# Kernel tuning notes

Measured on AMD Instinct MI355X. Metric: run time of the kernel, lower is better.

## Reference

```python
import jax, jax.numpy as jnp
import numpy as np

B = 4096
NUM_FEATURES = 2048
NUM_NEURONS = 1024
NUM_TARGETS = 8
NNZ1 = 65536
NNZ2 = 8192


def _sparse_linear(x, w, b, rows, cols, n_out):
    """y[b, o] = sum_{e: rows[e]==o} w[e] * x[b, cols[e]] + b[o].

    x: [B, n_in], w: [nnz], rows/cols: [nnz] int, b: [n_out].
    """
    prod = x[:, cols] * w  # [B, nnz] gather + elementwise
    # segment_sum reduces over leading axis -> work on [nnz, B]
    y = jax.ops.segment_sum(prod.T, rows, num_segments=n_out)  # [n_out, B]
    return y.T + b


def setup_inputs() -> dict:
    key = jax.random.key(0)
    ks = jax.random.split(key, 9)
    x = jax.random.normal(ks[0], (B, NUM_FEATURES), dtype=jnp.float32)
    w1 = jax.random.normal(ks[1], (NNZ1,), dtype=jnp.float32) * 0.05
    b1 = jax.random.normal(ks[2], (NUM_NEURONS,), dtype=jnp.float32) * 0.05
    w2 = jax.random.normal(ks[3], (NNZ2,), dtype=jnp.float32) * 0.05
    b2 = jax.random.normal(ks[4], (NUM_TARGETS,), dtype=jnp.float32) * 0.05
    conn1_out = jax.random.randint(ks[5], (NNZ1,), 0, NUM_NEURONS, dtype=jnp.int64 if jax.config.jax_enable_x64 else jnp.int32)
    conn1_in = jax.random.randint(ks[6], (NNZ1,), 0, NUM_FEATURES, dtype=conn1_out.dtype)
    conn2_out = jax.random.randint(ks[7], (NNZ2,), 0, NUM_TARGETS, dtype=conn1_out.dtype)
    conn2_in = jax.random.randint(ks[8], (NNZ2,), 0, NUM_NEURONS, dtype=conn1_out.dtype)
    return {
        "x": x, "w1": w1, "b1": b1, "w2": w2, "b2": b2,
        "conn1_out": conn1_out, "conn1_in": conn1_in,
        "conn2_out": conn2_out, "conn2_in": conn2_in,
    }


def reference(x, w1, b1, w2, b2, conn1_out, conn1_in, conn2_out, conn2_in):
    h = jax.nn.sigmoid(_sparse_linear(x, w1, b1, conn1_out, conn1_in, b1.shape[0]))
    out = _sparse_linear(h, w2, b2, conn2_out, conn2_in, b2.shape[0])
    # num_targets = 8 != 1, so no final sigmoid (matches CrossEntropyLoss path)
    return out
```

## Files before the change

kernel.cpp:

```cpp
#include <hip/hip_runtime.h>
#include <math.h>

#define BATCH 4096
#define NFEAT 2048
#define NNEUR 1024
#define NTGT  8
#define NNZ1  65536
#define NNZ2  8192

#define BM 128
#define BN 64
#define BK 64
#define KSTEPS (NFEAT / BK)

typedef short  bf16x8 __attribute__((ext_vector_type(8)));
typedef float  f32x4  __attribute__((ext_vector_type(4)));

#define OFF_W1F  ((size_t)0)
#define OFF_W2D  ((size_t)8388608)
#define OFF_W1B  ((size_t)8421376)

#define ZERO_FLOAT4 526336
#define OUT_FLOAT4  (BATCH * NTGT / 4)

__device__ __forceinline__ unsigned short f2bf(float f) {
    union { float f; unsigned int u; } a; a.f = f;
    unsigned int u = a.u;
    u += 0x7fffu + ((u >> 16) & 1u);
    return (unsigned short)(u >> 16);
}

__device__ __forceinline__ uint4 pk8(float4 lo, float4 hi) {
    uint4 r;
    asm("v_cvt_pk_bf16_f32 %0, %1, %2" : "=v"(r.x) : "v"(lo.x), "v"(lo.y));
    asm("v_cvt_pk_bf16_f32 %0, %1, %2" : "=v"(r.y) : "v"(lo.z), "v"(lo.w));
    asm("v_cvt_pk_bf16_f32 %0, %1, %2" : "=v"(r.z) : "v"(hi.x), "v"(hi.y));
    asm("v_cvt_pk_bf16_f32 %0, %1, %2" : "=v"(r.w) : "v"(hi.z), "v"(hi.w));
    return r;
}

__global__ void k_zero(float4* __restrict__ ws4, float4* __restrict__ out4,
                       const float* __restrict__ b2) {
    int i = blockIdx.x * blockDim.x + threadIdx.x;
    if (i < ZERO_FLOAT4) {
        ws4[i] = make_float4(0.f, 0.f, 0.f, 0.f);
    } else {
        int j = i - ZERO_FLOAT4;
        if (j < OUT_FLOAT4) {
            int p = (j & 1) * 4;
            out4[j] = make_float4(b2[p], b2[p + 1], b2[p + 2], b2[p + 3]);
        }
    }
}

__global__ void k_build(const float* __restrict__ w1, const int* __restrict__ c1o,
                        const int* __restrict__ c1i,
                        const float* __restrict__ w2, const int* __restrict__ c2o,
                        const int* __restrict__ c2i,
                        float* __restrict__ W1f, float* __restrict__ W2d) {
    int i = blockIdx.x * blockDim.x + threadIdx.x;
    if (i < NNZ1) {
        atomicAdd(&W1f[(size_t)c1o[i] * NFEAT + c1i[i]], w1[i]);
    } else {
        int j = i - NNZ1;
        if (j < NNZ2) atomicAdd(&W2d[c2i[j] * NTGT + c2o[j]], w2[j]);
    }
}

__global__ void k_convert(const float* __restrict__ W1f, unsigned short* __restrict__ W1b) {
    int i = blockIdx.x * blockDim.x + threadIdx.x;
    float4 v = ((const float4*)W1f)[i];
    ushort4 o;
    o.x = f2bf(v.x); o.y = f2bf(v.y); o.z = f2bf(v.z); o.w = f2bf(v.w);
    ((ushort4*)W1b)[i] = o;
}

__global__ __launch_bounds__(256) void k_gemm(const unsigned short* __restrict__ W1b,
                                              const float* __restrict__ x,
                                              const float* __restrict__ b1,
                                              const float* __restrict__ W2d,
                                              float* __restrict__ out) {
    __shared__ unsigned short ldsA[2][BM * BK];
    __shared__ unsigned short ldsB[2][BN * BK];
    __shared__ float s_w2[BM][NTGT];
    __shared__ float s_b1[BM];
    __shared__ float s_pt[2][BN][NTGT];

    int bid = blockIdx.x;
    int v   = bid >> 3;
    int n0  = ((bid & 7) * 8 + (v >> 3)) * BN;
    int mt  = v & 7;
    int m0  = mt * BM;

    int tid  = threadIdx.x;
    int wv   = tid >> 6;
    int lane = tid & 63;
    int wm = wv >> 1, wn = wv & 1;
    int lr = lane & 15, lg = lane >> 4;

    for (int i = tid; i < BM * NTGT; i += 256)
        s_w2[i >> 3][i & 7] = W2d[(m0 + (i >> 3)) * NTGT + (i & 7)];
    if (tid < BM) s_b1[tid] = b1[m0 + tid];

    f32x4 zero4 = {0.f, 0.f, 0.f, 0.f};
    f32x4 acc[4][2];
#pragma unroll
    for (int i = 0; i < 4; ++i)
#pragma unroll
        for (int j = 0; j < 2; ++j) acc[i][j] = zero4;

    int r0 = tid >> 3, s0 = tid & 7;
    const unsigned short* gA0 = &W1b[(size_t)(m0 + r0) * NFEAT + s0 * 8];
    const unsigned short* gA1 = gA0 + 32 * NFEAT;
    const unsigned short* gA2 = gA0 + 64 * NFEAT;
    const unsigned short* gA3 = gA0 + 96 * NFEAT;
    const float* gB0 = &x[(size_t)(n0 + r0) * NFEAT + s0 * 8];
    const float* gB1 = gB0 + 32 * NFEAT;
    const int iw0 = r0 * 8 + (s0 ^ (r0 & 7));
    const int iw1 = iw0 + 256, iw2 = iw0 + 512, iw3 = iw0 + 768;

    bf16x8 A0a, A0b, A0c, A0d;  float4 B0a, B0b, B0c, B0d;
    bf16x8 A1a, A1b, A1c, A1d;  float4 B1a, B1b, B1c, B1d;
    bf16x8 af0[4], af1[4], bg0[2], bg1[2];

#define LOADS0(T) do { int kk = (T) * BK;                           \
        A0a = *(const bf16x8*)(gA0 + kk); A0b = *(const bf16x8*)(gA1 + kk); \
        A0c = *(const bf16x8*)(gA2 + kk); A0d = *(const bf16x8*)(gA3 + kk); \
        B0a = *(const float4*)(gB0 + kk); B0b = *(const float4*)(gB0 + kk + 4); \
        B0c = *(const float4*)(gB1 + kk); B0d = *(const float4*)(gB1 + kk + 4); } while (0)
#define LOADS1(T) do { int kk = (T) * BK;                           \
        A1a = *(const bf16x8*)(gA0 + kk); A1b = *(const bf16x8*)(gA1 + kk); \
        A1c = *(const bf16x8*)(gA2 + kk); A1d = *(const bf16x8*)(gA3 + kk); \
        B1a = *(const float4*)(gB0 + kk); B1b = *(const float4*)(gB0 + kk + 4); \
        B1c = *(const float4*)(gB1 + kk); B1d = *(const float4*)(gB1 + kk + 4); } while (0)

#define STORE0(BUF) do {                                            \
        bf16x8* dA = (bf16x8*)&ldsA[BUF][0];                        \
        dA[iw0] = A0a; dA[iw1] = A0b; dA[iw2] = A0c; dA[iw3] = A0d; \
        uint4* dB = (uint4*)&ldsB[BUF][0];                          \
        dB[iw0] = pk8(B0a, B0b); dB[iw1] = pk8(B0c, B0d); } while (0)
#define STORE1(BUF) do {                                            \
        bf16x8* dA = (bf16x8*)&ldsA[BUF][0];                        \
        dA[iw0] = A1a; dA[iw1] = A1b; dA[iw2] = A1c; dA[iw3] = A1d; \
        uint4* dB = (uint4*)&ldsB[BUF][0];                          \
        dB[iw0] = pk8(B1a, B1b); dB[iw1] = pk8(B1c, B1d); } while (0)

#define READF(BUF) do {                                             \
        const unsigned short* bA = ldsA[BUF];                       \
        const unsigned short* bB = ldsB[BUF];                       \
        _Pragma("unroll")                                           \
        for (int i = 0; i < 4; ++i) {                               \
            int rowa = wm * 64 + i * 16 + lr;                       \
            af0[i] = *(const bf16x8*)&bA[(rowa * 8 + ((lg)     ^ (rowa & 7))) * 8]; \
            af1[i] = *(const bf16x8*)&bA[(rowa * 8 + ((4 + lg) ^ (rowa & 7))) * 8]; \
        }                                                           \
        _Pragma("unroll")                                           \
        for (int j = 0; j < 2; ++j) {                               \
            int rowb = wn * 32 + j * 16 + lr;                       \
            bg0[j] = *(const bf16x8*)&bB[(rowb * 8 + ((lg)     ^ (rowb & 7))) * 8]; \
            bg1[j] = *(const bf16x8*)&bB[(rowb * 8 + ((4 + lg) ^ (rowb & 7))) * 8]; \
        }                                                           \
    } while (0)

#define MFMAS() do {                                                \
        _Pragma("unroll")                                           \
        for (int i = 0; i < 4; ++i)                                 \
            _Pragma("unroll")                                       \
            for (int j = 0; j < 2; ++j)                             \
                acc[i][j] = __builtin_amdgcn_mfma_f32_16x16x32_bf16(af0[i], bg0[j], acc[i][j], 0, 0, 0); \
        _Pragma("unroll")                                           \
        for (int i = 0; i < 4; ++i)                                 \
            _Pragma("unroll")                                       \
            for (int j = 0; j < 2; ++j)                             \
                acc[i][j] = __builtin_amdgcn_mfma_f32_16x16x32_bf16(af1[i], bg1[j], acc[i][j], 0, 0, 0); \
    } while (0)

#define LDSFENCE() asm volatile("s_waitcnt lgkmcnt(0)" ::: "memory")

    LOADS0(0);
    LOADS1(1);
    STORE0(0);
    LDSFENCE();
    __builtin_amdgcn_s_barrier();

#pragma unroll 1
    for (int p = 0; p < 15; ++p) {
        int e = 2 * p;
        LOADS0(e + 2);
        STORE1(1);
        READF(0);
        MFMAS();
        LDSFENCE();
        __builtin_amdgcn_s_barrier();
        LOADS1(e + 3);
        STORE0(0);
        READF(1);
        MFMAS();
        LDSFENCE();
        __builtin_amdgcn_s_barrier();
    }
    STORE1(1);
    READF(0);
    MFMAS();
    LDSFENCE();
    __builtin_amdgcn_s_barrier();
    READF(1);
    MFMAS();

#undef LOADS0
#undef LOADS1
#undef STORE0
#undef STORE1
#undef READF
#undef MFMAS
#undef LDSFENCE

    float pt[2][NTGT];
#pragma unroll
    for (int j = 0; j < 2; ++j)
#pragma unroll
        for (int t = 0; t < NTGT; ++t) pt[j][t] = 0.f;

#pragma unroll
    for (int i = 0; i < 4; ++i) {
#pragma unroll
        for (int r = 0; r < 4; ++r) {
            int ml = wm * 64 + i * 16 + lg * 4 + r;
            float bn = s_b1[ml];
#pragma unroll
            for (int j = 0; j < 2; ++j) {
                float h = 1.f / (1.f + __expf(-(acc[i][j][r] + bn)));
#pragma unroll
                for (int t = 0; t < NTGT; ++t)
                    pt[j][t] += h * s_w2[ml][t];
            }
        }
    }
#pragma unroll
    for (int j = 0; j < 2; ++j)
#pragma unroll
        for (int t = 0; t < NTGT; ++t) {
            float val = pt[j][t];
            val += __shfl_xor(val, 16, 64);
            val += __shfl_xor(val, 32, 64);
            pt[j][t] = val;
        }
    if (lg == 0) {
#pragma unroll
        for (int j = 0; j < 2; ++j) {
            int nl = wn * 32 + j * 16 + lr;
#pragma unroll
            for (int t = 0; t < NTGT; ++t)
                s_pt[wm][nl][t] = pt[j][t];
        }
    }
    __syncthreads();
    for (int idx = tid; idx < BN * NTGT; idx += 256) {
        int nl = idx >> 3, t = idx & 7;
        atomicAdd(&out[(size_t)(n0 + nl) * NTGT + t], s_pt[0][nl][t] + s_pt[1][nl][t]);
    }
}

extern "C" void kernel_launch(void* const* d_in, const int* in_sizes, int n_in,
                              void* d_out, int out_size, void* d_ws, size_t ws_size,
                              hipStream_t stream) {
    (void)in_sizes; (void)n_in; (void)out_size; (void)ws_size;
    const float* x   = (const float*)d_in[0];
    const float* w1  = (const float*)d_in[1];
    const float* b1  = (const float*)d_in[2];
    const float* w2  = (const float*)d_in[3];
    const float* b2  = (const float*)d_in[4];
    const int*   c1o = (const int*)d_in[5];
    const int*   c1i = (const int*)d_in[6];
    const int*   c2o = (const int*)d_in[7];
    const int*   c2i = (const int*)d_in[8];
    float* out = (float*)d_out;

    char* ws = (char*)d_ws;
    float*          W1f  = (float*)(ws + OFF_W1F);
    float*          W2d  = (float*)(ws + OFF_W2D);
    unsigned short* W1b  = (unsigned short*)(ws + OFF_W1B);

    k_zero<<<(ZERO_FLOAT4 + OUT_FLOAT4 + 255) / 256, 256, 0, stream>>>(
        (float4*)ws, (float4*)out, b2);

    k_build<<<(NNZ1 + NNZ2) / 256, 256, 0, stream>>>(w1, c1o, c1i, w2, c2o, c2i, W1f, W2d);

    k_convert<<<NNEUR * NFEAT / 4 / 256, 256, 0, stream>>>(W1f, W1b);

    k_gemm<<<(NNEUR / BM) * (BATCH / BN), 256, 0, stream>>>(W1b, x, b1, W2d, out);
}
```

Before: 50.41 us.

## Pre-convert x to bf16 and enlarge GEMM tile to 128x128

The input x is now converted to bf16 once in the conversion kernel, so the GEMM loads bf16 directly instead of converting fp32 to bf16 per tile in every block. The N tile grows from 64 to 128, giving each wave a 4x4 MFMA accumulator block and halving the number of times W1 is re-read. The LDS staging for w2, b1 and partial outputs is dropped in favour of direct global loads and per-wave atomics. In exchange there is an extra pass over x (read fp32, write bf16), only 256 blocks are launched, register pressure is higher, and more atomics hit the output.

```diff
diff --git a/kernel.cpp b/kernel.cpp
--- a/kernel.cpp
+++ b/kernel.cpp
@@ -9,7 +9,7 @@
 #define NNZ2  8192
 
 #define BM 128
-#define BN 64
+#define BN 128
 #define BK 64
 #define KSTEPS (NFEAT / BK)
 
@@ -19,6 +19,7 @@
 #define OFF_W1F  ((size_t)0)
 #define OFF_W2D  ((size_t)8388608)
 #define OFF_W1B  ((size_t)8421376)
+#define OFF_XB   ((size_t)12615680)
 
 #define ZERO_FLOAT4 526336
 #define OUT_FLOAT4  (BATCH * NTGT / 4)
@@ -28,15 +29,6 @@
     unsigned int u = a.u;
     u += 0x7fffu + ((u >> 16) & 1u);
     return (unsigned short)(u >> 16);
-}
-
-__device__ __forceinline__ uint4 pk8(float4 lo, float4 hi) {
-    uint4 r;
-    asm("v_cvt_pk_bf16_f32 %0, %1, %2" : "=v"(r.x) : "v"(lo.x), "v"(lo.y));
-    asm("v_cvt_pk_bf16_f32 %0, %1, %2" : "=v"(r.y) : "v"(lo.z), "v"(lo.w));
-    asm("v_cvt_pk_bf16_f32 %0, %1, %2" : "=v"(r.z) : "v"(hi.x), "v"(hi.y));
-    asm("v_cvt_pk_bf16_f32 %0, %1, %2" : "=v"(r.w) : "v"(hi.z), "v"(hi.w));
-    return r;
 }
 
 __global__ void k_zero(float4* __restrict__ ws4, float4* __restrict__ out4,
@@ -67,30 +59,38 @@
     }
 }
 
-__global__ void k_convert(const float* __restrict__ W1f, unsigned short* __restrict__ W1b) {
+__global__ void k_convert(const float* __restrict__ W1f, const float* __restrict__ x,
+                          unsigned short* __restrict__ W1b, unsigned short* __restrict__ xb) {
     int i = blockIdx.x * blockDim.x + threadIdx.x;
-    float4 v = ((const float4*)W1f)[i];
-    ushort4 o;
-    o.x = f2bf(v.x); o.y = f2bf(v.y); o.z = f2bf(v.z); o.w = f2bf(v.w);
-    ((ushort4*)W1b)[i] = o;
+    const int nW = NNEUR * NFEAT / 4;
+    const int nX = BATCH * NFEAT / 4;
+    if (i < nW) {
+        float4 v = ((const float4*)W1f)[i];
+        ushort4 o;
+        o.x = f2bf(v.x); o.y = f2bf(v.y); o.z = f2bf(v.z); o.w = f2bf(v.w);
+        ((ushort4*)W1b)[i] = o;
+    } else if (i < nW + nX) {
+        int j = i - nW;
+        float4 v = ((const float4*)x)[j];
+        ushort4 o;
+        o.x = f2bf(v.x); o.y = f2bf(v.y); o.z = f2bf(v.z); o.w = f2bf(v.w);
+        ((ushort4*)xb)[j] = o;
+    }
 }
 
 __global__ __launch_bounds__(256) void k_gemm(const unsigned short* __restrict__ W1b,
-                                              const float* __restrict__ x,
+                                              const unsigned short* __restrict__ xb,
                                               const float* __restrict__ b1,
                                               const float* __restrict__ W2d,
                                               float* __restrict__ out) {
     __shared__ unsigned short ldsA[2][BM * BK];
     __shared__ unsigned short ldsB[2][BN * BK];
-    __shared__ float s_w2[BM][NTGT];
-    __shared__ float s_b1[BM];
-    __shared__ float s_pt[2][BN][NTGT];
-
-    int bid = blockIdx.x;
-    int v   = bid >> 3;
-    int n0  = ((bid & 7) * 8 + (v >> 3)) * BN;
-    int mt  = v & 7;
-    int m0  = mt * BM;
+
+    int bid  = blockIdx.x;
+    int virt = (bid & 7) * 32 + (bid >> 3);
+    int n0 = (virt >> 3) * BN;
+    int mt = virt & 7;
+    int m0 = mt * BM;
 
     int tid  = threadIdx.x;
     int wv   = tid >> 6;
@@ -98,82 +98,68 @@
     int wm = wv >> 1, wn = wv & 1;
     int lr = lane & 15, lg = lane >> 4;
 
-    for (int i = tid; i < BM * NTGT; i += 256)
-        s_w2[i >> 3][i & 7] = W2d[(m0 + (i >> 3)) * NTGT + (i & 7)];
-    if (tid < BM) s_b1[tid] = b1[m0 + tid];
-
-    f32x4 zero4 = {0.f, 0.f, 0.f, 0.f};
-    f32x4 acc[4][2];
+    f32x4 acc[4][4];
 #pragma unroll
     for (int i = 0; i < 4; ++i)
 #pragma unroll
-        for (int j = 0; j < 2; ++j) acc[i][j] = zero4;
+        for (int j = 0; j < 4; ++j) acc[i][j] = (f32x4){0.f, 0.f, 0.f, 0.f};
 
     int r0 = tid >> 3, s0 = tid & 7;
     const unsigned short* gA0 = &W1b[(size_t)(m0 + r0) * NFEAT + s0 * 8];
     const unsigned short* gA1 = gA0 + 32 * NFEAT;
     const unsigned short* gA2 = gA0 + 64 * NFEAT;
     const unsigned short* gA3 = gA0 + 96 * NFEAT;
-    const float* gB0 = &x[(size_t)(n0 + r0) * NFEAT + s0 * 8];
-    const float* gB1 = gB0 + 32 * NFEAT;
+    const unsigned short* gB0 = &xb[(size_t)(n0 + r0) * NFEAT + s0 * 8];
+    const unsigned short* gB1 = gB0 + 32 * NFEAT;
+    const unsigned short* gB2 = gB0 + 64 * NFEAT;
+    const unsigned short* gB3 = gB0 + 96 * NFEAT;
     const int iw0 = r0 * 8 + (s0 ^ (r0 & 7));
     const int iw1 = iw0 + 256, iw2 = iw0 + 512, iw3 = iw0 + 768;
 
-    bf16x8 A0a, A0b, A0c, A0d;  float4 B0a, B0b, B0c, B0d;
-    bf16x8 A1a, A1b, A1c, A1d;  float4 B1a, B1b, B1c, B1d;
-    bf16x8 af0[4], af1[4], bg0[2], bg1[2];
+    bf16x8 A0a, A0b, A0c, A0d, B0a, B0b, B0c, B0d;
+    bf16x8 A1a, A1b, A1c, A1d, B1a, B1b, B1c, B1d;
+    bf16x8 af[4], bg[4];
 
 #define LOADS0(T) do { int kk = (T) * BK;                           \
         A0a = *(const bf16x8*)(gA0 + kk); A0b = *(const bf16x8*)(gA1 + kk); \
         A0c = *(const bf16x8*)(gA2 + kk); A0d = *(const bf16x8*)(gA3 + kk); \
-        B0a = *(const float4*)(gB0 + kk); B0b = *(const float4*)(gB0 + kk + 4); \
-        B0c = *(const float4*)(gB1 + kk); B0d = *(const float4*)(gB1 + kk + 4); } while (0)
+        B0a = *(const bf16x8*)(gB0 + kk); B0b = *(const bf16x8*)(gB1 + kk); \
+        B0c = *(const bf16x8*)(gB2 + kk); B0d = *(const bf16x8*)(gB3 + kk); } while (0)
 #define LOADS1(T) do { int kk = (T) * BK;                           \
         A1a = *(const bf16x8*)(gA0 + kk); A1b = *(const bf16x8*)(gA1 + kk); \
         A1c = *(const bf16x8*)(gA2 + kk); A1d = *(const bf16x8*)(gA3 + kk); \
-        B1a = *(const float4*)(gB0 + kk); B1b = *(const float4*)(gB0 + kk + 4); \
-        B1c = *(const float4*)(gB1 + kk); B1d = *(const float4*)(gB1 + kk + 4); } while (0)
+        B1a = *(const bf16x8*)(gB0 + kk); B1b = *(const bf16x8*)(gB1 + kk); \
+        B1c = *(const bf16x8*)(gB2 + kk); B1d = *(const bf16x8*)(gB3 + kk); } while (0)
 
 #define STORE0(BUF) do {                                            \
         bf16x8* dA = (bf16x8*)&ldsA[BUF][0];                        \
+        bf16x8* dB = (bf16x8*)&ldsB[BUF][0];                        \
         dA[iw0] = A0a; dA[iw1] = A0b; dA[iw2] = A0c; dA[iw3] = A0d; \
-        uint4* dB = (uint4*)&ldsB[BUF][0];                          \
-        dB[iw0] = pk8(B0a, B0b); dB[iw1] = pk8(B0c, B0d); } while (0)
+        dB[iw0] = B0a; dB[iw1] = B0b; dB[iw2] = B0c; dB[iw3] = B0d; } while (0)
 #define STORE1(BUF) do {                                            \
         bf16x8* dA = (bf16x8*)&ldsA[BUF][0];                        \
+        bf16x8* dB = (bf16x8*)&ldsB[BUF][0];                        \
         dA[iw0] = A1a; dA[iw1] = A1b; dA[iw2] = A1c; dA[iw3] = A1d; \
-        uint4* dB = (uint4*)&ldsB[BUF][0];                          \
-        dB[iw0] = pk8(B1a, B1b); dB[iw1] = pk8(B1c, B1d); } while (0)
-
-#define READF(BUF) do {                                             \
+        dB[iw0] = B1a; dB[iw1] = B1b; dB[iw2] = B1c; dB[iw3] = B1d; } while (0)
+
+#define HALF(BUF, KS) do {                                          \
         const unsigned short* bA = ldsA[BUF];                       \
         const unsigned short* bB = ldsB[BUF];                       \
         _Pragma("unroll")                                           \
-        for (int i = 0; i < 4; ++i) {                               \
-            int rowa = wm * 64 + i * 16 + lr;                       \
-            af0[i] = *(const bf16x8*)&bA[(rowa * 8 + ((lg)     ^ (rowa & 7))) * 8]; \
-            af1[i] = *(const bf16x8*)&bA[(rowa * 8 + ((4 + lg) ^ (rowa & 7))) * 8]; \
+        for (int f = 0; f < 4; ++f) {                               \
+            int ra = wm * 64 + f * 16 + lr;                         \
+            af[f] = *(const bf16x8*)&bA[(ra * 8 + (((KS) * 4 + lg) ^ (ra & 7))) * 8]; \
+            int rb = wn * 64 + f * 16 + lr;                         \
+            bg[f] = *(const bf16x8*)&bB[(rb * 8 + (((KS) * 4 + lg) ^ (rb & 7))) * 8]; \
         }                                                           \
-        _Pragma("unroll")                                           \
-        for (int j = 0; j < 2; ++j) {                               \
-            int rowb = wn * 32 + j * 16 + lr;                       \
-            bg0[j] = *(const bf16x8*)&bB[(rowb * 8 + ((lg)     ^ (rowb & 7))) * 8]; \
-            bg1[j] = *(const bf16x8*)&bB[(rowb * 8 + ((4 + lg) ^ (rowb & 7))) * 8]; \
-        }                                                           \
-    } while (0)
-
-#define MFMAS() do {                                                \
         _Pragma("unroll")                                           \
         for (int i = 0; i < 4; ++i)                                 \
             _Pragma("unroll")                                       \
-            for (int j = 0; j < 2; ++j)                             \
-                acc[i][j] = __builtin_amdgcn_mfma_f32_16x16x32_bf16(af0[i], bg0[j], acc[i][j], 0, 0, 0); \
-        _Pragma("unroll")                                           \
-        for (int i = 0; i < 4; ++i)                                 \
-            _Pragma("unroll")                                       \
-            for (int j = 0; j < 2; ++j)                             \
-                acc[i][j] = __builtin_amdgcn_mfma_f32_16x16x32_bf16(af1[i], bg1[j], acc[i][j], 0, 0, 0); \
+            for (int j = 0; j < 4; ++j)                             \
+                acc[i][j] = __builtin_amdgcn_mfma_f32_16x16x32_bf16(af[i], bg[j], acc[i][j], 0, 0, 0); \
     } while (0)
+
+#define COMPUTE(BUF) do { HALF(BUF, 0); HALF(BUF, 1); } while (0)
 
 #define LDSFENCE() asm volatile("s_waitcnt lgkmcnt(0)" ::: "memory")
 
@@ -188,36 +174,32 @@
         int e = 2 * p;
         LOADS0(e + 2);
         STORE1(1);
-        READF(0);
-        MFMAS();
+        COMPUTE(0);
         LDSFENCE();
         __builtin_amdgcn_s_barrier();
         LOADS1(e + 3);
         STORE0(0);
-        READF(1);
-        MFMAS();
+        COMPUTE(1);
         LDSFENCE();
         __builtin_amdgcn_s_barrier();
     }
     STORE1(1);
-    READF(0);
-    MFMAS();
+    COMPUTE(0);
     LDSFENCE();
     __builtin_amdgcn_s_barrier();
-    READF(1);
-    MFMAS();
+    COMPUTE(1);
 
 #undef LOADS0
 #undef LOADS1
 #undef STORE0
 #undef STORE1
-#undef READF
-#undef MFMAS
+#undef HALF
+#undef COMPUTE
 #undef LDSFENCE
 
-    float pt[2][NTGT];
-#pragma unroll
-    for (int j = 0; j < 2; ++j)
+    float pt[4][NTGT];
+#pragma unroll
+    for (int j = 0; j < 4; ++j)
 #pragma unroll
         for (int t = 0; t < NTGT; ++t) pt[j][t] = 0.f;
 
@@ -225,19 +207,22 @@
     for (int i = 0; i < 4; ++i) {
 #pragma unroll
         for (int r = 0; r < 4; ++r) {
-            int ml = wm * 64 + i * 16 + lg * 4 + r;
-            float bn = s_b1[ml];
-#pragma unroll
-            for (int j = 0; j < 2; ++j) {
+            int m = m0 + wm * 64 + i * 16 + lg * 4 + r;
+            float bn = b1[m];
+            float4 w2lo = *(const float4*)&W2d[m * NTGT];
+            float4 w2hi = *(const float4*)&W2d[m * NTGT + 4];
+#pragma unroll
+            for (int j = 0; j < 4; ++j) {
                 float h = 1.f / (1.f + __expf(-(acc[i][j][r] + bn)));
-#pragma unroll
-                for (int t = 0; t < NTGT; ++t)
-                    pt[j][t] += h * s_w2[ml][t];
+                pt[j][0] += h * w2lo.x; pt[j][1] += h * w2lo.y;
+                pt[j][2] += h * w2lo.z; pt[j][3] += h * w2lo.w;
+                pt[j][4] += h * w2hi.x; pt[j][5] += h * w2hi.y;
+                pt[j][6] += h * w2hi.z; pt[j][7] += h * w2hi.w;
             }
         }
     }
 #pragma unroll
-    for (int j = 0; j < 2; ++j)
+    for (int j = 0; j < 4; ++j)
 #pragma unroll
         for (int t = 0; t < NTGT; ++t) {
             float val = pt[j][t];
@@ -247,17 +232,12 @@
         }
     if (lg == 0) {
 #pragma unroll
-        for (int j = 0; j < 2; ++j) {
-            int nl = wn * 32 + j * 16 + lr;
+        for (int j = 0; j < 4; ++j) {
+            int n = n0 + wn * 64 + j * 16 + lr;
 #pragma unroll
             for (int t = 0; t < NTGT; ++t)
-                s_pt[wm][nl][t] = pt[j][t];
-        }
-    }
-    __syncthreads();
-    for (int idx = tid; idx < BN * NTGT; idx += 256) {
-        int nl = idx >> 3, t = idx & 7;
-        atomicAdd(&out[(size_t)(n0 + nl) * NTGT + t], s_pt[0][nl][t] + s_pt[1][nl][t]);
+                atomicAdd(&out[(size_t)n * NTGT + t], pt[j][t]);
+        }
     }
 }
 
@@ -280,13 +260,14 @@
     float*          W1f  = (float*)(ws + OFF_W1F);
     float*          W2d  = (float*)(ws + OFF_W2D);
     unsigned short* W1b  = (unsigned short*)(ws + OFF_W1B);
+    unsigned short* xb   = (unsigned short*)(ws + OFF_XB);
 
     k_zero<<<(ZERO_FLOAT4 + OUT_FLOAT4 + 255) / 256, 256, 0, stream>>>(
         (float4*)ws, (float4*)out, b2);
 
     k_build<<<(NNZ1 + NNZ2) / 256, 256, 0, stream>>>(w1, c1o, c1i, w2, c2o, c2i, W1f, W2d);
 
-    k_convert<<<NNEUR * NFEAT / 4 / 256, 256, 0, stream>>>(W1f, W1b);
-
-    k_gemm<<<(NNEUR / BM) * (BATCH / BN), 256, 0, stream>>>(W1b, x, b1, W2d, out);
-}
+    k_convert<<<(NNEUR * NFEAT / 4 + BATCH * NFEAT / 4) / 256, 256, 0, stream>>>(W1f, x, W1b, xb);
+
+    k_gemm<<<(NNEUR / BM) * (BATCH / BN), 256, 0, stream>>>(W1b, xb, b1, W2d, out);
+}
```

New measurement: 72.91 us. 44.7% more time.
